# Performance work log

Hardware: AMD Instinct MI355X
Metric: run time of the kernel (lower is better)

The kernel has to match this reference:

```python
import jax, jax.numpy as jnp
import numpy as np

B, W, K = 8, 200, 100   # batch, window_size, n_features
KS = 7                   # conv kernel size
HID = 150                # GRU hidden dim
ALPHA = 0.2              # leaky relu slope
FE = 2 * W               # feature GAT embed dim (gatv2 doubles window_size)
TE = 2 * K               # temporal GAT embed dim (gatv2 doubles n_features)


def setup_inputs() -> dict:
    key = jax.random.key(0)
    ks = jax.random.split(key, 16)
    s = lambda k, shape, sc=0.05: jax.random.normal(k, shape, jnp.float32) * sc
    return {
        "x": jax.random.normal(ks[0], (B, W, K), jnp.float32),
        "conv_w": s(ks[1], (K, K, KS)),
        "conv_b": s(ks[2], (K,)),
        "f_lin_w": s(ks[3], (2 * W, FE)),
        "f_lin_b": s(ks[4], (FE,)),
        "f_a": s(ks[5], (FE,)),
        "f_bias": s(ks[6], (K, K)),
        "t_lin_w": s(ks[7], (2 * K, TE)),
        "t_lin_b": s(ks[8], (TE,)),
        "t_a": s(ks[9], (TE,)),
        "t_bias": s(ks[10], (W, W)),
        "w_ih": s(ks[11], (3 * HID, 3 * K)),
        "w_hh": s(ks[12], (3 * HID, HID)),
        "b_ih": s(ks[13], (3 * HID,)),
        "b_hh": s(ks[14], (3 * HID,)),
    }


def _leaky(x):
    return jnp.where(x >= 0, x, ALPHA * x)


def _gatv2(v, lin_w, lin_b, a, bias):
    """GATv2 layer over fully-connected graph. v: (b, N, D).
    e_ij = a . leakyrelu(W [v_i || v_j] + b_lin); out = sigmoid(softmax(e+bias) @ v).
    Splitting W rows avoids materializing the (b,N,N,2D) concat tensor."""
    D = v.shape[-1]
    w1, w2 = lin_w[:D], lin_w[D:]
    si = jnp.einsum('bnd,de->bne', v, w1)  # contribution of node i (repeated)
    sj = jnp.einsum('bnd,de->bne', v, w2)  # contribution of node j (alternating)
    g = _leaky(si[:, :, None, :] + sj[:, None, :, :] + lin_b)  # (b,N,N,E)
    e = jnp.einsum('bije,e->bij', g, a) + bias                 # (b,N,N)
    attn = jax.nn.softmax(e, axis=2)
    return jax.nn.sigmoid(jnp.einsum('bij,bjd->bid', attn, v))  # (b,N,D)


def _forward(x, conv_w, conv_b, f_lin_w, f_lin_b, f_a, f_bias,
             t_lin_w, t_lin_b, t_a, t_bias, w_ih, w_hh, b_ih, b_hh):
    # ConvLayer: permute to (b,K,W), pad 3 both sides, conv1d k=7, relu, permute back
    xc = jnp.transpose(x, (0, 2, 1))
    xc = jax.lax.conv_general_dilated(xc, conv_w, (1,), [((KS - 1) // 2, (KS - 1) // 2)],
                                      dimension_numbers=('NCH', 'OIH', 'NCH'))
    xc = jax.nn.relu(xc + conv_b[None, :, None])
    xc = jnp.transpose(xc, (0, 2, 1))  # (b, W, K)

    # Feature GAT: nodes = features, per-node vector = window
    h_feat = _gatv2(jnp.transpose(xc, (0, 2, 1)), f_lin_w, f_lin_b, f_a, f_bias)
    h_feat = jnp.transpose(h_feat, (0, 2, 1))  # (b, W, K)
    # Temporal GAT: nodes = timesteps, per-node vector = features
    h_temp = _gatv2(xc, t_lin_w, t_lin_b, t_a, t_bias)  # (b, W, K)

    h_cat = jnp.concatenate([xc, h_feat, h_temp], axis=2)  # (b, W, 3K)

    # Single-layer GRU, torch gate order (r, z, n), batch_first; return final hidden
    def step(h, xt):
        gi = xt @ w_ih.T + b_ih
        gh = h @ w_hh.T + b_hh
        ir, iz, inn = jnp.split(gi, 3, axis=-1)
        hr, hz, hn = jnp.split(gh, 3, axis=-1)
        r = jax.nn.sigmoid(ir + hr)
        z = jax.nn.sigmoid(iz + hz)
        n = jnp.tanh(inn + r * hn)
        return (1.0 - z) * n + z * h, None

    h0 = jnp.zeros((x.shape[0], HID), x.dtype)
    h_end, _ = jax.lax.scan(step, h0, jnp.transpose(h_cat, (1, 0, 2)))
    return h_end  # (b, HID)


def reference(x, conv_w, conv_b, f_lin_w, f_lin_b, f_a, f_bias,
              t_lin_w, t_lin_b, t_a, t_bias, w_ih, w_hh, b_ih, b_hh):
    return _forward(x, conv_w, conv_b, f_lin_w, f_lin_b, f_a, f_bias,
                    t_lin_w, t_lin_b, t_a, t_bias, w_ih, w_hh, b_ih, b_hh)
```

## Files before the change

kernel.cpp:

```cpp
#include <hip/hip_runtime.h>
#include <math.h>

#define NB   8
#define NW   200
#define NK   100
#define KSZ  7
#define NHID 150
#define NFE  400
#define NTE  200
#define NG   450
#define NCIN 300
#define ALPHAC 0.2f

__device__ __forceinline__ float sigmoidf_(float x){
  return 1.0f/(1.0f + __expf(-x));
}
__device__ __forceinline__ float tanhf_(float x){
  float xc = fminf(fmaxf(x, -15.f), 15.f);
  float e = __expf(2.f*xc);
  return (e - 1.f)/(e + 1.f);
}

__global__ void prep_kernel(const float* conv_w, const float* w_ih, const float* w_hh,
                            float* conv_wT, float* w_ihT, float* w_hhT){
  int idx = blockIdx.x*256 + threadIdx.x;
  const int n1 = NK*NK*KSZ;
  const int n2 = NG*NCIN;
  const int n3 = 150*512;
  if (idx < n1){
    int k = idx % NK; int it = idx / NK;
    int i = it / KSZ, t = it % KSZ;
    conv_wT[idx] = conv_w[(k*NK + i)*KSZ + t];
  } else if (idx < n1 + n2){
    int o = idx - n1; int g = o % NG; int c = o / NG;
    w_ihT[o] = w_ih[g*NCIN + c];
  } else if (idx < n1 + n2 + n3){
    int o = idx - n1 - n2; int g = o % 512; int j = o / 512;
    w_hhT[o] = (g < NG) ? w_hh[g*NHID + j] : 0.f;
  }
}

__global__ void conv_kernel(const float* x, const float* conv_b, const float* conv_wT, float* xc){
  int idx = blockIdx.x*256 + threadIdx.x;
  if (idx >= NB*NW*NK) return;
  int k = idx % NK; int w = (idx/NK) % NW; int b = idx/(NK*NW);
  float acc = conv_b[k];
  const float* xb = x + b*NW*NK;
  for (int t = 0; t < KSZ; ++t){
    int ws = w + t - 3;
    if (ws < 0 || ws >= NW) continue;
    const float* xr = xb + ws*NK;
    const float* wr = conv_wT + t*NK + k;
    #pragma unroll 4
    for (int i = 0; i < NK; ++i){
      acc += xr[i] * wr[i*KSZ*NK];
    }
  }
  xc[idx] = fmaxf(acc, 0.0f);
}

__global__ void fgat_sisj(const float* xc, const float* f_lin_w, float* si, float* sj){
  __shared__ __align__(16) float vt[NW*4];
  int b = blockIdx.x / 25; int n0 = (blockIdx.x % 25)*4;
  int tid = threadIdx.x;
  for (int idx = tid; idx < NW*4; idx += 512){
    int d = idx >> 2, nn = idx & 3;
    vt[idx] = xc[(b*NW + d)*NK + n0 + nn];
  }
  __syncthreads();
  if (tid >= NFE) return;
  int e = tid;
  float a1[4] = {0,0,0,0}, a2[4] = {0,0,0,0};
  for (int d = 0; d < NW; ++d){
    float w1 = f_lin_w[d*NFE + e];
    float w2 = f_lin_w[(NW + d)*NFE + e];
    float4 v = *(const float4*)&vt[d*4];
    a1[0] += v.x*w1; a1[1] += v.y*w1; a1[2] += v.z*w1; a1[3] += v.w*w1;
    a2[0] += v.x*w2; a2[1] += v.y*w2; a2[2] += v.z*w2; a2[3] += v.w*w2;
  }
  #pragma unroll
  for (int nn = 0; nn < 4; ++nn){
    si[(b*NK + n0+nn)*NFE + e] = a1[nn];
    sj[(b*NK + n0+nn)*NFE + e] = a2[nn];
  }
}

__global__ void tgat_sisj(const float* xc, const float* t_lin_w, float* si, float* sj){
  __shared__ __align__(16) float vt[NK*4];
  int b = blockIdx.x / 50; int n0 = (blockIdx.x % 50)*4;
  int tid = threadIdx.x;
  for (int idx = tid; idx < NK*4; idx += 256){
    int d = idx >> 2, nn = idx & 3;
    vt[idx] = xc[(b*NW + n0+nn)*NK + d];
  }
  __syncthreads();
  if (tid >= NTE) return;
  int e = tid;
  float a1[4] = {0,0,0,0}, a2[4] = {0,0,0,0};
  for (int d = 0; d < NK; ++d){
    float w1 = t_lin_w[d*NTE + e];
    float w2 = t_lin_w[(NK + d)*NTE + e];
    float4 v = *(const float4*)&vt[d*4];
    a1[0] += v.x*w1; a1[1] += v.y*w1; a1[2] += v.z*w1; a1[3] += v.w*w1;
    a2[0] += v.x*w2; a2[1] += v.y*w2; a2[2] += v.z*w2; a2[3] += v.w*w2;
  }
  #pragma unroll
  for (int nn = 0; nn < 4; ++nn){
    si[(b*NW + n0+nn)*NTE + e] = a1[nn];
    sj[(b*NW + n0+nn)*NTE + e] = a2[nn];
  }
}

__global__ void fgat_attn(const float* xc, const float* si, const float* sj,
                          const float* f_lin_b, const float* f_a, const float* f_bias,
                          float* h_featT){
  __shared__ float sib[NFE], av[NFE], attn[NK], red[128];
  int b = blockIdx.x / NK, i = blockIdx.x % NK;
  int tid = threadIdx.x;
  for (int e = tid; e < NFE; e += 128){
    sib[e] = si[(b*NK + i)*NFE + e] + f_lin_b[e];
    av[e]  = f_a[e];
  }
  __syncthreads();
  float ej = -1e30f;
  if (tid < NK){
    const float* sjr = sj + (b*NK + tid)*NFE;
    float acc = 0.f;
    for (int e = 0; e < NFE; ++e){
      float tv = sib[e] + sjr[e];
      float lk = fmaxf(tv, 0.f) + ALPHAC*fminf(tv, 0.f);
      acc += av[e]*lk;
    }
    ej = acc + f_bias[i*NK + tid];
  }
  red[tid] = ej; __syncthreads();
  for (int s = 64; s > 0; s >>= 1){ if (tid < s) red[tid] = fmaxf(red[tid], red[tid+s]); __syncthreads(); }
  float m = red[0]; __syncthreads();
  float ex = (tid < NK) ? __expf(ej - m) : 0.f;
  red[tid] = ex; __syncthreads();
  for (int s = 64; s > 0; s >>= 1){ if (tid < s) red[tid] += red[tid+s]; __syncthreads(); }
  float denom = red[0];
  if (tid < NK) attn[tid] = ex / denom;
  __syncthreads();
  for (int d = tid; d < NW; d += 128){
    const float* xr = xc + (b*NW + d)*NK;
    float acc = 0.f;
    for (int j = 0; j < NK; ++j) acc += attn[j]*xr[j];
    h_featT[(b*NW + d)*NK + i] = sigmoidf_(acc);
  }
}

__global__ void tgat_attn(const float* xc, const float* si, const float* sj,
                          const float* t_lin_b, const float* t_a, const float* t_bias,
                          float* h_temp){
  __shared__ float sib[NTE], av[NTE], attn[NW], red[256];
  int b = blockIdx.x / NW, i = blockIdx.x % NW;
  int tid = threadIdx.x;
  for (int e = tid; e < NTE; e += 256){
    sib[e] = si[(b*NW + i)*NTE + e] + t_lin_b[e];
    av[e]  = t_a[e];
  }
  __syncthreads();
  float ej = -1e30f;
  if (tid < NW){
    const float* sjr = sj + (b*NW + tid)*NTE;
    float acc = 0.f;
    for (int e = 0; e < NTE; ++e){
      float tv = sib[e] + sjr[e];
      float lk = fmaxf(tv, 0.f) + ALPHAC*fminf(tv, 0.f);
      acc += av[e]*lk;
    }
    ej = acc + t_bias[i*NW + tid];
  }
  red[tid] = ej; __syncthreads();
  for (int s = 128; s > 0; s >>= 1){ if (tid < s) red[tid] = fmaxf(red[tid], red[tid+s]); __syncthreads(); }
  float m = red[0]; __syncthreads();
  float ex = (tid < NW) ? __expf(ej - m) : 0.f;
  red[tid] = ex; __syncthreads();
  for (int s = 128; s > 0; s >>= 1){ if (tid < s) red[tid] += red[tid+s]; __syncthreads(); }
  float denom = red[0];
  if (tid < NW) attn[tid] = ex / denom;
  __syncthreads();
  for (int d = tid; d < NK; d += 256){
    float acc = 0.f;
    for (int j = 0; j < NW; ++j) acc += attn[j]*xc[(b*NW + j)*NK + d];
    h_temp[(b*NW + i)*NK + d] = sigmoidf_(acc);
  }
}

__global__ void gi_kernel(const float* xc, const float* h_featT, const float* h_temp,
                          const float* w_ihT, const float* b_ih, float* gi){
  __shared__ __align__(16) float hc[NCIN*8];
  int b = blockIdx.x / 25; int t0 = (blockIdx.x % 25)*8;
  int tid = threadIdx.x;
  for (int idx = tid; idx < NCIN*8; idx += 512){
    int tt = idx / NCIN; int c = idx % NCIN;
    int base = (b*NW + t0 + tt)*NK;
    float v;
    if (c < NK)        v = xc[base + c];
    else if (c < 2*NK) v = h_featT[base + c - NK];
    else               v = h_temp[base + c - 2*NK];
    hc[c*8 + tt] = v;
  }
  __syncthreads();
  if (tid >= NG) return;
  int g = tid;
  float bi = b_ih[g];
  float acc[8];
  #pragma unroll
  for (int tt = 0; tt < 8; ++tt) acc[tt] = bi;
  for (int c = 0; c < NCIN; ++c){
    float wv = w_ihT[c*NG + g];
    float4 h0 = *(const float4*)&hc[c*8];
    float4 h1 = *(const float4*)&hc[c*8+4];
    acc[0] += h0.x*wv; acc[1] += h0.y*wv; acc[2] += h0.z*wv; acc[3] += h0.w*wv;
    acc[4] += h1.x*wv; acc[5] += h1.y*wv; acc[6] += h1.z*wv; acc[7] += h1.w*wv;
  }
  #pragma unroll
  for (int tt = 0; tt < 8; ++tt)
    gi[((t0+tt)*NB + b)*NG + g] = acc[tt];
}

__global__ void __launch_bounds__(512, 2) gru_kernel(const float* gi, const float* w_hhT,
                                                     const float* b_hh, float* out){
  __shared__ __align__(16) float h[152];
  __shared__ float gh[512];
  int b = blockIdx.x; int tid = threadIdx.x;
  int gsafe = (tid < NG) ? tid : 0;
  float bh = b_hh[gsafe];
  float wreg[152];
  #pragma unroll
  for (int j = 0; j < 150; ++j)
    wreg[j] = w_hhT[j*512 + tid];
  wreg[150] = 0.f; wreg[151] = 0.f;
  if (tid < 152) h[tid] = 0.f;
  __syncthreads();
  for (int t = 0; t < NW; ++t){
    float p0 = 0.f, p1 = 0.f, p2 = 0.f;
    if (tid < NHID){
      const float* gir = gi + (t*NB + b)*NG;
      p0 = gir[tid]; p1 = gir[NHID + tid]; p2 = gir[2*NHID + tid];
    }
    float acc = bh;
    #pragma unroll
    for (int j4 = 0; j4 < 38; ++j4){
      float4 hv = *(const float4*)&h[j4*4];
      acc += wreg[j4*4+0]*hv.x + wreg[j4*4+1]*hv.y
           + wreg[j4*4+2]*hv.z + wreg[j4*4+3]*hv.w;
    }
    gh[tid] = acc;
    __syncthreads();
    if (tid < NHID){
      float r = sigmoidf_(p0 + gh[tid]);
      float z = sigmoidf_(p1 + gh[NHID + tid]);
      float n = tanhf_  (p2 + r*gh[2*NHID + tid]);
      h[tid] = (1.f - z)*n + z*h[tid];
    }
    __syncthreads();
  }
  if (tid < NHID) out[b*NHID + tid] = h[tid];
}

extern "C" void kernel_launch(void* const* d_in, const int* in_sizes, int n_in,
                              void* d_out, int out_size, void* d_ws, size_t ws_size,
                              hipStream_t stream){
  const float* x       = (const float*)d_in[0];
  const float* conv_w  = (const float*)d_in[1];
  const float* conv_b  = (const float*)d_in[2];
  const float* f_lin_w = (const float*)d_in[3];
  const float* f_lin_b = (const float*)d_in[4];
  const float* f_a     = (const float*)d_in[5];
  const float* f_bias  = (const float*)d_in[6];
  const float* t_lin_w = (const float*)d_in[7];
  const float* t_lin_b = (const float*)d_in[8];
  const float* t_a     = (const float*)d_in[9];
  const float* t_bias  = (const float*)d_in[10];
  const float* w_ih    = (const float*)d_in[11];
  const float* w_hh    = (const float*)d_in[12];
  const float* b_ih    = (const float*)d_in[13];
  const float* b_hh    = (const float*)d_in[14];

  float* ws      = (float*)d_ws;
  float* xc      = ws;
  float* conv_wT = ws + 160000;
  float* si_f    = ws + 230000;
  float* sj_f    = ws + 550000;
  float* h_featT = ws + 870000;
  float* si_t    = ws + 1030000;
  float* sj_t    = ws + 1350000;
  float* h_temp  = ws + 1670000;
  float* w_ihT   = ws + 1830000;
  float* gi      = ws + 1965000;
  float* w_hhT   = ws + 2685000;

  prep_kernel<<<1101, 256, 0, stream>>>(conv_w, w_ih, w_hh, conv_wT, w_ihT, w_hhT);
  conv_kernel<<<(NB*NW*NK + 255)/256, 256, 0, stream>>>(x, conv_b, conv_wT, xc);
  fgat_sisj<<<NB*25, 512, 0, stream>>>(xc, f_lin_w, si_f, sj_f);
  tgat_sisj<<<NB*50, 256, 0, stream>>>(xc, t_lin_w, si_t, sj_t);
  fgat_attn<<<NB*NK, 128, 0, stream>>>(xc, si_f, sj_f, f_lin_b, f_a, f_bias, h_featT);
  tgat_attn<<<NB*NW, 256, 0, stream>>>(xc, si_t, sj_t, t_lin_b, t_a, t_bias, h_temp);
  gi_kernel<<<NB*25, 512, 0, stream>>>(xc, h_featT, h_temp, w_ihT, b_ih, gi);
  gru_kernel<<<NB, 512, 0, stream>>>(gi, w_hhT, b_hh, (float*)d_out);
}
```

Measured before the change: 425.2 us.

## Split GRU hidden matvec across two thread halves with 1024-thread blocks

```diff
diff --git a/kernel.cpp b/kernel.cpp
--- a/kernel.cpp
+++ b/kernel.cpp
@@ -22,11 +22,11 @@
 }
 
 __global__ void prep_kernel(const float* conv_w, const float* w_ih, const float* w_hh,
-                            float* conv_wT, float* w_ihT, float* w_hhT){
+                            float* conv_wT, float* w_ihT, float* w_hhPad){
   int idx = blockIdx.x*256 + threadIdx.x;
   const int n1 = NK*NK*KSZ;
   const int n2 = NG*NCIN;
-  const int n3 = 150*512;
+  const int n3 = 152*512;
   if (idx < n1){
     int k = idx % NK; int it = idx / NK;
     int i = it / KSZ, t = it % KSZ;
@@ -36,7 +36,7 @@
     w_ihT[o] = w_ih[g*NCIN + c];
   } else if (idx < n1 + n2 + n3){
     int o = idx - n1 - n2; int g = o % 512; int j = o / 512;
-    w_hhT[o] = (g < NG) ? w_hh[g*NHID + j] : 0.f;
+    w_hhPad[o] = (g < NG && j < NHID) ? w_hh[g*NHID + j] : 0.f;
   }
 }
 
@@ -221,18 +221,23 @@
     gi[((t0+tt)*NB + b)*NG + g] = acc[tt];
 }
 
-__global__ void __launch_bounds__(512, 2) gru_kernel(const float* gi, const float* w_hhT,
-                                                     const float* b_hh, float* out){
+__global__ void __launch_bounds__(1024, 4) gru_kernel(const float* gi, const float* w_hhPad,
+                                                      const float* b_hh, float* out){
   __shared__ __align__(16) float h[152];
-  __shared__ float gh[512];
+  __shared__ float part[1024];
   int b = blockIdx.x; int tid = threadIdx.x;
-  int gsafe = (tid < NG) ? tid : 0;
-  float bh = b_hh[gsafe];
-  float wreg[152];
-  #pragma unroll
-  for (int j = 0; j < 150; ++j)
-    wreg[j] = w_hhT[j*512 + tid];
-  wreg[150] = 0.f; wreg[151] = 0.f;
+  int g = tid & 511; int half = tid >> 9;
+  int jbase = half*76;
+  float bh = (half == 0 && g < NG) ? b_hh[g] : 0.f;
+  float4 wreg[19];
+  #pragma unroll
+  for (int jj = 0; jj < 19; ++jj){
+    int j = jbase + jj*4;
+    wreg[jj].x = w_hhPad[(j+0)*512 + g];
+    wreg[jj].y = w_hhPad[(j+1)*512 + g];
+    wreg[jj].z = w_hhPad[(j+2)*512 + g];
+    wreg[jj].w = w_hhPad[(j+3)*512 + g];
+  }
   if (tid < 152) h[tid] = 0.f;
   __syncthreads();
   for (int t = 0; t < NW; ++t){
@@ -243,17 +248,20 @@
     }
     float acc = bh;
     #pragma unroll
-    for (int j4 = 0; j4 < 38; ++j4){
-      float4 hv = *(const float4*)&h[j4*4];
-      acc += wreg[j4*4+0]*hv.x + wreg[j4*4+1]*hv.y
-           + wreg[j4*4+2]*hv.z + wreg[j4*4+3]*hv.w;
-    }
-    gh[tid] = acc;
+    for (int jj = 0; jj < 19; ++jj){
+      float4 hv = *(const float4*)&h[jbase + jj*4];
+      acc += wreg[jj].x*hv.x + wreg[jj].y*hv.y
+           + wreg[jj].z*hv.z + wreg[jj].w*hv.w;
+    }
+    part[tid] = acc;
     __syncthreads();
     if (tid < NHID){
-      float r = sigmoidf_(p0 + gh[tid]);
-      float z = sigmoidf_(p1 + gh[NHID + tid]);
-      float n = tanhf_  (p2 + r*gh[2*NHID + tid]);
+      float ghr = part[tid]       + part[512 + tid];
+      float ghz = part[150 + tid] + part[512 + 150 + tid];
+      float ghn = part[300 + tid] + part[512 + 300 + tid];
+      float r = sigmoidf_(p0 + ghr);
+      float z = sigmoidf_(p1 + ghz);
+      float n = tanhf_  (p2 + r*ghn);
       h[tid] = (1.f - z)*n + z*h[tid];
     }
     __syncthreads();
@@ -291,14 +299,14 @@
   float* h_temp  = ws + 1670000;
   float* w_ihT   = ws + 1830000;
   float* gi      = ws + 1965000;
-  float* w_hhT   = ws + 2685000;
-
-  prep_kernel<<<1101, 256, 0, stream>>>(conv_w, w_ih, w_hh, conv_wT, w_ihT, w_hhT);
+  float* w_hhPad = ws + 2685000;
+
+  prep_kernel<<<1105, 256, 0, stream>>>(conv_w, w_ih, w_hh, conv_wT, w_ihT, w_hhPad);
   conv_kernel<<<(NB*NW*NK + 255)/256, 256, 0, stream>>>(x, conv_b, conv_wT, xc);
   fgat_sisj<<<NB*25, 512, 0, stream>>>(xc, f_lin_w, si_f, sj_f);
   tgat_sisj<<<NB*50, 256, 0, stream>>>(xc, t_lin_w, si_t, sj_t);
   fgat_attn<<<NB*NK, 128, 0, stream>>>(xc, si_f, sj_f, f_lin_b, f_a, f_bias, h_featT);
   tgat_attn<<<NB*NW, 256, 0, stream>>>(xc, si_t, sj_t, t_lin_b, t_a, t_bias, h_temp);
   gi_kernel<<<NB*25, 512, 0, stream>>>(xc, h_featT, h_temp, w_ihT, b_ih, gi);
-  gru_kernel<<<NB, 512, 0, stream>>>(gi, w_hhT, b_hh, (float*)d_out);
-}
+  gru_kernel<<<NB, 1024, 0, stream>>>(gi, w_hhPad, b_hh, (float*)d_out);
+}
```

New measurement: 391.3 us. 8.0% less time.

## Run GRU recurrence in one block using bf16 MFMA with split-precision hidden state

Applied to the files above, without the earlier changes.

```diff
diff --git a/kernel.cpp b/kernel.cpp
--- a/kernel.cpp
+++ b/kernel.cpp
@@ -12,6 +12,9 @@
 #define NCIN 300
 #define ALPHAC 0.2f
 
+typedef __attribute__((ext_vector_type(8))) short bf8;
+typedef __attribute__((ext_vector_type(4))) float f32x4;
+
 __device__ __forceinline__ float sigmoidf_(float x){
   return 1.0f/(1.0f + __expf(-x));
 }
@@ -20,13 +23,18 @@
   float e = __expf(2.f*xc);
   return (e - 1.f)/(e + 1.f);
 }
+__device__ __forceinline__ unsigned short f2bf(float f){
+  unsigned int u = __float_as_uint(f);
+  unsigned int r = u + 0x7FFFu + ((u>>16)&1u);
+  return (unsigned short)(r>>16);
+}
 
 __global__ void prep_kernel(const float* conv_w, const float* w_ih, const float* w_hh,
-                            float* conv_wT, float* w_ihT, float* w_hhT){
+                            float* conv_wT, float* w_ihT, unsigned int* Bfrag){
   int idx = blockIdx.x*256 + threadIdx.x;
   const int n1 = NK*NK*KSZ;
   const int n2 = NG*NCIN;
-  const int n3 = 150*512;
+  const int n3 = 32*5*64*4;
   if (idx < n1){
     int k = idx % NK; int it = idx / NK;
     int i = it / KSZ, t = it % KSZ;
@@ -35,8 +43,21 @@
     int o = idx - n1; int g = o % NG; int c = o / NG;
     w_ihT[o] = w_ih[g*NCIN + c];
   } else if (idx < n1 + n2 + n3){
-    int o = idx - n1 - n2; int g = o % 512; int j = o / 512;
-    w_hhT[o] = (g < NG) ? w_hh[g*NHID + j] : 0.f;
+    int o = idx - n1 - n2;
+    int n   = o / 1280;
+    int rem = o % 1280;
+    int ks  = rem / 256;
+    int rem2= rem % 256;
+    int l   = rem2 >> 2;
+    int d   = rem2 & 3;
+    int col = n*16 + (l & 15);
+    int k0  = ks*32 + (l >> 4)*8 + d*2;
+    unsigned short lo = 0, hi = 0;
+    if (col < NG){
+      if (k0     < NHID) lo = f2bf(w_hh[col*NHID + k0]);
+      if (k0 + 1 < NHID) hi = f2bf(w_hh[col*NHID + k0 + 1]);
+    }
+    Bfrag[o] = ((unsigned int)hi << 16) | lo;
   }
 }
 
@@ -221,44 +242,127 @@
     gi[((t0+tt)*NB + b)*NG + g] = acc[tt];
 }
 
-__global__ void __launch_bounds__(512, 2) gru_kernel(const float* gi, const float* w_hhT,
+#define MM(C, A, Bf) C = __builtin_amdgcn_mfma_f32_16x16x32_bf16(A, Bf, C, 0, 0, 0);
+#define TILE_MM(C, K0,K1,K2,K3,K4) \
+  MM(C,aH0,K0) MM(C,aL0,K0) MM(C,aH1,K1) MM(C,aL1,K1) MM(C,aH2,K2) MM(C,aL2,K2) \
+  MM(C,aH3,K3) MM(C,aL3,K3) MM(C,aH4,K4) MM(C,aL4,K4)
+#define LDB(NM, TL, KS) bf8 NM = Bfrag[((TL)*5 + (KS))*64 + lane];
+
+__global__ void __launch_bounds__(512, 2) gru_kernel(const float* gi, const bf8* Bfrag,
                                                      const float* b_hh, float* out){
-  __shared__ __align__(16) float h[152];
-  __shared__ float gh[512];
-  int b = blockIdx.x; int tid = threadIdx.x;
-  int gsafe = (tid < NG) ? tid : 0;
-  float bh = b_hh[gsafe];
-  float wreg[152];
-  #pragma unroll
-  for (int j = 0; j < 150; ++j)
-    wreg[j] = w_hhT[j*512 + tid];
-  wreg[150] = 0.f; wreg[151] = 0.f;
-  if (tid < 152) h[tid] = 0.f;
-  __syncthreads();
+  __shared__ __align__(16) unsigned short h_hi[16*176];
+  __shared__ __align__(16) unsigned short h_lo[16*176];
+  __shared__ __align__(16) float h_f32[8*152];
+  __shared__ __align__(16) float gh[16*516];
+  int tid = threadIdx.x;
+  int lane = tid & 63;
+  int wv = tid >> 6;
+  int agrp = lane >> 4;
+  int arow = lane & 15;
+  int crow = agrp*4;
+  int ccol = arow;
+
+  int p0 = tid, p1 = tid + 512, p2 = tid + 1024;
+  int b0 = p0/NHID, u0 = p0%NHID;
+  int b1 = p1/NHID, u1 = p1%NHID;
+  bool v2 = (p2 < NB*NHID);
+  int b2 = v2 ? p2/NHID : 0, u2 = v2 ? p2%NHID : 0;
+  float bhr0 = b_hh[u0],      bhz0 = b_hh[NHID+u0],  bhn0 = b_hh[2*NHID+u0];
+  float bhr1 = b_hh[u1],      bhz1 = b_hh[NHID+u1],  bhn1 = b_hh[2*NHID+u1];
+  float bhr2 = b_hh[u2],      bhz2 = b_hh[NHID+u2],  bhn2 = b_hh[2*NHID+u2];
+
+  LDB(W00,wv,0)    LDB(W01,wv,1)    LDB(W02,wv,2)    LDB(W03,wv,3)    LDB(W04,wv,4)
+  LDB(W10,wv+8,0)  LDB(W11,wv+8,1)  LDB(W12,wv+8,2)  LDB(W13,wv+8,3)  LDB(W14,wv+8,4)
+  LDB(W20,wv+16,0) LDB(W21,wv+16,1) LDB(W22,wv+16,2) LDB(W23,wv+16,3) LDB(W24,wv+16,4)
+  LDB(W30,wv+24,0) LDB(W31,wv+24,1) LDB(W32,wv+24,2) LDB(W33,wv+24,3) LDB(W34,wv+24,4)
+
+  for (int i = tid; i < 16*176; i += 512){ h_hi[i] = 0; h_lo[i] = 0; }
+  for (int i = tid; i < 8*152;  i += 512){ h_f32[i] = 0.f; }
+  __syncthreads();
+
+  const bf8* HH = (const bf8*)h_hi;
+  const bf8* HL = (const bf8*)h_lo;
+  int abase = arow*22 + agrp;
+
   for (int t = 0; t < NW; ++t){
-    float p0 = 0.f, p1 = 0.f, p2 = 0.f;
-    if (tid < NHID){
-      const float* gir = gi + (t*NB + b)*NG;
-      p0 = gir[tid]; p1 = gir[NHID + tid]; p2 = gir[2*NHID + tid];
-    }
-    float acc = bh;
-    #pragma unroll
-    for (int j4 = 0; j4 < 38; ++j4){
-      float4 hv = *(const float4*)&h[j4*4];
-      acc += wreg[j4*4+0]*hv.x + wreg[j4*4+1]*hv.y
-           + wreg[j4*4+2]*hv.z + wreg[j4*4+3]*hv.w;
-    }
-    gh[tid] = acc;
+    const float* gt = gi + t*NB*NG;
+    float gr0 = gt[b0*NG+u0], gz0 = gt[b0*NG+NHID+u0], gn0 = gt[b0*NG+2*NHID+u0];
+    float gr1 = gt[b1*NG+u1], gz1 = gt[b1*NG+NHID+u1], gn1 = gt[b1*NG+2*NHID+u1];
+    float gr2 = 0.f, gz2 = 0.f, gn2 = 0.f;
+    if (v2){ gr2 = gt[b2*NG+u2]; gz2 = gt[b2*NG+NHID+u2]; gn2 = gt[b2*NG+2*NHID+u2]; }
+
+    bf8 aH0 = HH[abase],    aH1 = HH[abase+4],  aH2 = HH[abase+8],
+        aH3 = HH[abase+12], aH4 = HH[abase+16];
+    bf8 aL0 = HL[abase],    aL1 = HL[abase+4],  aL2 = HL[abase+8],
+        aL3 = HL[abase+12], aL4 = HL[abase+16];
+
+    f32x4 c0 = {0.f,0.f,0.f,0.f}, c1 = {0.f,0.f,0.f,0.f},
+          c2 = {0.f,0.f,0.f,0.f}, c3 = {0.f,0.f,0.f,0.f};
+    TILE_MM(c0, W00,W01,W02,W03,W04)
+    TILE_MM(c1, W10,W11,W12,W13,W14)
+    TILE_MM(c2, W20,W21,W22,W23,W24)
+    TILE_MM(c3, W30,W31,W32,W33,W34)
+
+    if (agrp < 2){
+      float* g0 = &gh[crow*516 + (wv   )*16 + ccol];
+      float* g1 = &gh[crow*516 + (wv+ 8)*16 + ccol];
+      float* g2 = &gh[crow*516 + (wv+16)*16 + ccol];
+      float* g3 = &gh[crow*516 + (wv+24)*16 + ccol];
+      g0[0]=c0[0]; g0[516]=c0[1]; g0[1032]=c0[2]; g0[1548]=c0[3];
+      g1[0]=c1[0]; g1[516]=c1[1]; g1[1032]=c1[2]; g1[1548]=c1[3];
+      g2[0]=c2[0]; g2[516]=c2[1]; g2[1032]=c2[2]; g2[1548]=c2[3];
+      g3[0]=c3[0]; g3[516]=c3[1]; g3[1032]=c3[2]; g3[1548]=c3[3];
+    }
     __syncthreads();
-    if (tid < NHID){
-      float r = sigmoidf_(p0 + gh[tid]);
-      float z = sigmoidf_(p1 + gh[NHID + tid]);
-      float n = tanhf_  (p2 + r*gh[2*NHID + tid]);
-      h[tid] = (1.f - z)*n + z*h[tid];
+
+    {
+      float r = sigmoidf_(gr0 + gh[b0*516+u0] + bhr0);
+      float z = sigmoidf_(gz0 + gh[b0*516+NHID+u0] + bhz0);
+      float n = tanhf_  (gn0 + r*(gh[b0*516+2*NHID+u0] + bhn0));
+      float hold = h_f32[b0*152+u0];
+      float hn = (1.f - z)*n + z*hold;
+      h_f32[b0*152+u0] = hn;
+      unsigned int ub = __float_as_uint(hn);
+      unsigned int hi = (ub + 0x7FFFu + ((ub>>16)&1u)) >> 16;
+      h_hi[b0*176+u0] = (unsigned short)hi;
+      float lo = hn - __uint_as_float(hi<<16);
+      unsigned int ul = __float_as_uint(lo);
+      h_lo[b0*176+u0] = (unsigned short)((ul + 0x7FFFu + ((ul>>16)&1u)) >> 16);
+    }
+    {
+      float r = sigmoidf_(gr1 + gh[b1*516+u1] + bhr1);
+      float z = sigmoidf_(gz1 + gh[b1*516+NHID+u1] + bhz1);
+      float n = tanhf_  (gn1 + r*(gh[b1*516+2*NHID+u1] + bhn1));
+      float hold = h_f32[b1*152+u1];
+      float hn = (1.f - z)*n + z*hold;
+      h_f32[b1*152+u1] = hn;
+      unsigned int ub = __float_as_uint(hn);
+      unsigned int hi = (ub + 0x7FFFu + ((ub>>16)&1u)) >> 16;
+      h_hi[b1*176+u1] = (unsigned short)hi;
+      float lo = hn - __uint_as_float(hi<<16);
+      unsigned int ul = __float_as_uint(lo);
+      h_lo[b1*176+u1] = (unsigned short)((ul + 0x7FFFu + ((ul>>16)&1u)) >> 16);
+    }
+    if (v2){
+      float r = sigmoidf_(gr2 + gh[b2*516+u2] + bhr2);
+      float z = sigmoidf_(gz2 + gh[b2*516+NHID+u2] + bhz2);
+      float n = tanhf_  (gn2 + r*(gh[b2*516+2*NHID+u2] + bhn2));
+      float hold = h_f32[b2*152+u2];
+      float hn = (1.f - z)*n + z*hold;
+      h_f32[b2*152+u2] = hn;
+      unsigned int ub = __float_as_uint(hn);
+      unsigned int hi = (ub + 0x7FFFu + ((ub>>16)&1u)) >> 16;
+      h_hi[b2*176+u2] = (unsigned short)hi;
+      float lo = hn - __uint_as_float(hi<<16);
+      unsigned int ul = __float_as_uint(lo);
+      h_lo[b2*176+u2] = (unsigned short)((ul + 0x7FFFu + ((ul>>16)&1u)) >> 16);
     }
     __syncthreads();
   }
-  if (tid < NHID) out[b*NHID + tid] = h[tid];
+
+  out[b0*NHID + u0] = h_f32[b0*152 + u0];
+  out[b1*NHID + u1] = h_f32[b1*152 + u1];
+  if (v2) out[b2*NHID + u2] = h_f32[b2*152 + u2];
 }
 
 extern "C" void kernel_launch(void* const* d_in, const int* in_sizes, int n_in,
@@ -291,14 +395,14 @@
   float* h_temp  = ws + 1670000;
   float* w_ihT   = ws + 1830000;
   float* gi      = ws + 1965000;
-  float* w_hhT   = ws + 2685000;
-
-  prep_kernel<<<1101, 256, 0, stream>>>(conv_w, w_ih, w_hh, conv_wT, w_ihT, w_hhT);
+  float* BfragF  = ws + 2685000;
+
+  prep_kernel<<<961, 256, 0, stream>>>(conv_w, w_ih, w_hh, conv_wT, w_ihT, (unsigned int*)BfragF);
   conv_kernel<<<(NB*NW*NK + 255)/256, 256, 0, stream>>>(x, conv_b, conv_wT, xc);
   fgat_sisj<<<NB*25, 512, 0, stream>>>(xc, f_lin_w, si_f, sj_f);
   tgat_sisj<<<NB*50, 256, 0, stream>>>(xc, t_lin_w, si_t, sj_t);
   fgat_attn<<<NB*NK, 128, 0, stream>>>(xc, si_f, sj_f, f_lin_b, f_a, f_bias, h_featT);
   tgat_attn<<<NB*NW, 256, 0, stream>>>(xc, si_t, sj_t, t_lin_b, t_a, t_bias, h_temp);
   gi_kernel<<<NB*25, 512, 0, stream>>>(xc, h_featT, h_temp, w_ihT, b_ih, gi);
-  gru_kernel<<<NB, 512, 0, stream>>>(gi, w_hhT, b_hh, (float*)d_out);
-}
+  gru_kernel<<<1, 512, 0, stream>>>(gi, (const bf8*)BfragF, b_hh, (float*)d_out);
+}
```

New measurement: 478.1 us. 12.4% more time.
